# Kernel optimization log

Hardware: AMD Instinct MI355X
Metric: run time of the kernel (lower is better)

Reference implementation:

```python
import jax, jax.numpy as jnp
import numpy as np

WIN = 7  # skimage structural_similarity default win_size


def _uniform_valid(x):
    # x: [N, H, W] -> [N, H-6, W-6]; 7x7 uniform (box) filter, VALID.
    # exactly equivalent to uniform_filter + crop (boundary mode irrelevant).
    k = jnp.ones((1, 1, WIN, WIN), x.dtype) / (WIN * WIN)
    y = jax.lax.conv_general_dilated(x[:, None], k, (1, 1), 'VALID')
    return y[:, 0]


def _ssim_frames(x, y):
    # K1=0.01, K2=0.03, data_range=255, sample covariance (N/(N-1)).
    C1 = (0.01 * 255.0) ** 2
    C2 = (0.03 * 255.0) ** 2
    NP = WIN * WIN
    cov_norm = NP / (NP - 1.0)
    ux = _uniform_valid(x)
    uy = _uniform_valid(y)
    uxx = _uniform_valid(x * x)
    uyy = _uniform_valid(y * y)
    uxy = _uniform_valid(x * y)
    vx = cov_norm * (uxx - ux * ux)
    vy = cov_norm * (uyy - uy * uy)
    vxy = cov_norm * (uxy - ux * uy)
    S = ((2.0 * ux * uy + C1) * (2.0 * vxy + C2)) / (
        (ux * ux + uy * uy + C1) * (vx + vy + C2))
    return jnp.mean(S, axis=(1, 2))  # per-frame mean SSIM


def setup_inputs() -> dict:
    key = jax.random.key(0)
    k1, k2, k3 = jax.random.split(key, 3)
    B, T, C, H, W = 8, 20, 1, 512, 512
    gen_img = jax.random.uniform(k1, (B, T, C, H, W), dtype=jnp.float32)
    target = jax.random.uniform(k2, (B, T, C, H, W), dtype=jnp.float32)
    gen_D = jax.random.normal(k3, (B, 1), dtype=jnp.float32)
    return {"gen_img": gen_img, "target": target, "gen_D": gen_D}


def reference(gen_img, target, gen_D):
    B, T, C, H, W = gen_img.shape
    diff = gen_img - target
    L_rec = jnp.mean(jnp.abs(diff)) + jnp.mean(diff * diff)
    # SSIM on channel 0 of every frame, scaled by 255 (as in the numpy loop);
    # original detaches, so stop_gradient for faithfulness.
    x = gen_img[:, :, 0].reshape(B * T, H, W) * 255.0
    y = target[:, :, 0].reshape(B * T, H, W) * 255.0
    L_ssim = jnp.mean(jax.lax.stop_gradient(_ssim_frames(x, y)))
    L_adv = -jnp.mean(gen_D)
    L_total = L_rec + 0.01 * (1.0 - L_ssim) + 0.0001 * L_adv
    return (L_total, L_rec, L_ssim, L_adv)
```

## Files before the change

### kernel.cpp

```cpp
#include <hip/hip_runtime.h>

#define FRAMES 160
#define HH 512
#define WW 512
#define STRIPS 16
#define NBLK (STRIPS * FRAMES)
#define NTOT 41943040

__device__ __forceinline__ void sync_lds() {
  __builtin_amdgcn_s_waitcnt(0xC07F);
  __builtin_amdgcn_s_barrier();
}

__device__ __forceinline__ float ssim_fast(float a, float b, float sxx,
                                           float syy, float sxy) {
  const float K1 = 0.2401f;
  const float K2 = 2.1609f;
  const float cA = 49.0f / 24.0f;
  const float cB = 49.0f / 48.0f;
  float ab = a * b;
  float s2 = fmaf(a, a, b * b);
  float A1 = fmaf(2.0f, ab, K1);
  float B1 = s2 + K1;
  float A2 = fmaf(cA, fmaf(49.0f, sxy, -ab), K2);
  float B2 = fmaf(cB, fmaf(49.0f, sxx + syy, -s2), K2);
  return (A1 * A2) * __builtin_amdgcn_rcpf(B1 * B2);
}

#define HSTORE(S, P, A)                          \
  P.x = S.x; P.y = P.x + S.y;                    \
  P.z = P.y + S.z; P.w = P.z + S.w;              \
  lds[grp][A][0][q] = make_float2(P.x, P.y);     \
  lds[grp][A][1][q] = make_float2(P.z, P.w);

#define HWIN(P, W, A) {                          \
  float2 h1 = lds[grp][A][1][q + 1];             \
  float2 l2 = lds[grp][A][0][q + 2];             \
  W.x = P.w + h1.x;                              \
  W.y = (P.w - P.x) + h1.y;                      \
  W.z = (P.w - P.y) + (h1.y + l2.x);             \
  W.w = (P.w - P.z) + (h1.y + l2.y); }

#define LREC(xv, yv) {                                         \
  float4 d_ = make_float4(xv.x - yv.x, xv.y - yv.y,            \
                          xv.z - yv.z, xv.w - yv.w);           \
  sabs += fabsf(d_.x) + fabsf(d_.y) + fabsf(d_.z) + fabsf(d_.w); \
  ssq += d_.x * d_.x + d_.y * d_.y;                            \
  ssq += d_.z * d_.z + d_.w * d_.w; }

#define VADD(xv, yv)                                    \
  Sx += xv; Sy += yv;                                   \
  Sxx += xv * xv; Syy += yv * yv; Sxy += xv * yv;

#define VSUB(xv, yv)                                    \
  Sx -= xv; Sy -= yv;                                   \
  Sxx -= xv * xv; Syy -= yv * yv; Sxy -= xv * yv;

__global__ __launch_bounds__(256, 4) void fused_kernel(
    const float* __restrict__ gsrc, const float* __restrict__ tsrc,
    float* __restrict__ ws) {
  const int strip = blockIdx.x;
  const int frame = blockIdx.y;
  const int row0 = strip * 32;
  const int n_iter = (strip == STRIPS - 1) ? 13 : 16;
  const int tid = threadIdx.x;
  const int grp = tid >> 7;
  const int q = tid & 127;

  const float* gp = gsrc + ((size_t)frame * HH + row0 + grp) * WW + q * 4;
  const float* tp = tsrc + ((size_t)frame * HH + row0 + grp) * WW + q * 4;

  __shared__ float2 lds[2][5][2][132];

  float4 Sx = make_float4(0.f, 0.f, 0.f, 0.f);
  float4 Sy = Sx, Sxx = Sx, Syy = Sx, Sxy = Sx;
  float sabs = 0.f, ssq = 0.f, ssum = 0.f;

  for (int i = 0; i < 7; ++i) {
    float4 xv = *(const float4*)(gp + i * WW);
    float4 yv = *(const float4*)(tp + i * WW);
    VADD(xv, yv)
    if (grp == 0) { LREC(xv, yv) }
  }

  for (int it = 0; it < n_iter; ++it) {
    const bool slide = (it + 1 < n_iter);
    float4 nx0, ny0, nx1, ny1, ox0, oy0, ox1, oy1;
    if (slide) {
      const float* pn = gp + (size_t)(2 * it + 7) * WW;
      const float* qn = tp + (size_t)(2 * it + 7) * WW;
      const float* po = gp + (size_t)(2 * it) * WW;
      const float* qo = tp + (size_t)(2 * it) * WW;
      nx0 = *(const float4*)pn;
      ny0 = *(const float4*)qn;
      nx1 = *(const float4*)(pn + WW);
      ny1 = *(const float4*)(qn + WW);
      ox0 = *(const float4*)po;
      oy0 = *(const float4*)qo;
      ox1 = *(const float4*)(po + WW);
      oy1 = *(const float4*)(qo + WW);
    }

    float4 Px, Py, Pxx, Pyy, Pxy;
    HSTORE(Sx, Px, 0) HSTORE(Sy, Py, 1) HSTORE(Sxx, Pxx, 2)
    HSTORE(Syy, Pyy, 3) HSTORE(Sxy, Pxy, 4)
    sync_lds();
    float4 Wx, Wy, Wxx, Wyy, Wxy;
    HWIN(Px, Wx, 0) HWIN(Py, Wy, 1) HWIN(Pxx, Wxx, 2)
    HWIN(Pyy, Wyy, 3) HWIN(Pxy, Wxy, 4)
    float v0 = ssim_fast(Wx.x, Wy.x, Wxx.x, Wyy.x, Wxy.x);
    float v1 = ssim_fast(Wx.y, Wy.y, Wxx.y, Wyy.y, Wxy.y);
    float v2 = ssim_fast(Wx.z, Wy.z, Wxx.z, Wyy.z, Wxy.z);
    float v3 = ssim_fast(Wx.w, Wy.w, Wxx.w, Wyy.w, Wxy.w);
    ssum += (q <= 126) ? v0 : 0.f;
    ssum += (q <= 126) ? v1 : 0.f;
    ssum += (q <= 125) ? v2 : 0.f;
    ssum += (q <= 125) ? v3 : 0.f;
    sync_lds();

    if (slide) {
      VADD(nx0, ny0)
      VSUB(ox0, oy0)
      if ((grp == 0) && (2 * it + 7 <= 30)) { LREC(nx0, ny0) }
      VADD(nx1, ny1)
      VSUB(ox1, oy1)
      bool cnt = (grp == 0) ? (2 * it + 8 <= 30) : (2 * it + 9 == 31);
      if (cnt) { LREC(nx1, ny1) }
    }
  }

  #pragma unroll
  for (int off = 32; off > 0; off >>= 1) {
    sabs += __shfl_down(sabs, off, 64);
    ssq += __shfl_down(ssq, off, 64);
    ssum += __shfl_down(ssum, off, 64);
  }
  __syncthreads();
  float* scr = (float*)&lds[0][0][0][0];
  const int lane = tid & 63, wv = tid >> 6;
  if (lane == 0) { scr[wv] = sabs; scr[4 + wv] = ssq; scr[8 + wv] = ssum; }
  __syncthreads();
  if (tid == 0) {
    const int bid = blockIdx.y * STRIPS + blockIdx.x;
    ws[bid] = scr[0] + scr[1] + scr[2] + scr[3];
    ws[NBLK + bid] = scr[4] + scr[5] + scr[6] + scr[7];
    ws[2 * NBLK + bid] = scr[8] + scr[9] + scr[10] + scr[11];
  }
}

__global__ __launch_bounds__(256) void finalize_kernel(
    const float* __restrict__ ws, const float* __restrict__ genD,
    float* __restrict__ out) {
  const int tid = threadIdx.x;
  float a = 0.f, b = 0.f, c = 0.f;
  for (int i = tid; i < NBLK; i += 256) {
    a += ws[i];
    b += ws[NBLK + i];
    c += ws[2 * NBLK + i];
  }
  #pragma unroll
  for (int off = 32; off > 0; off >>= 1) {
    a += __shfl_down(a, off, 64);
    b += __shfl_down(b, off, 64);
    c += __shfl_down(c, off, 64);
  }
  __shared__ float la[4], lb[4], lc[4];
  const int lane = tid & 63, wv = tid >> 6;
  if (lane == 0) { la[wv] = a; lb[wv] = b; lc[wv] = c; }
  __syncthreads();
  if (tid == 0) {
    a = la[0] + la[1] + la[2] + la[3];
    b = lb[0] + lb[1] + lb[2] + lb[3];
    c = lc[0] + lc[1] + lc[2] + lc[3];
    const float invN = 1.0f / (float)NTOT;
    float L_rec = a * invN + b * invN;
    float L_ssim = c / (160.0f * 506.0f * 506.0f);
    float d = 0.f;
    #pragma unroll
    for (int i = 0; i < 8; ++i) d += genD[i];
    float L_adv = -d / 8.0f;
    float L_total = L_rec + 0.01f * (1.0f - L_ssim) + 0.0001f * L_adv;
    out[0] = L_total;
    out[1] = L_rec;
    out[2] = L_ssim;
    out[3] = L_adv;
  }
}

extern "C" void kernel_launch(void* const* d_in, const int* in_sizes, int n_in,
                              void* d_out, int out_size, void* d_ws,
                              size_t ws_size, hipStream_t stream) {
  const float* gen_img = (const float*)d_in[0];
  const float* target = (const float*)d_in[1];
  const float* gen_D = (const float*)d_in[2];
  float* out = (float*)d_out;
  float* ws = (float*)d_ws;

  dim3 grid(STRIPS, FRAMES);
  fused_kernel<<<grid, 256, 0, stream>>>(gen_img, target, ws);
  finalize_kernel<<<1, 256, 0, stream>>>(ws, gen_D, out);
}
```

Before: 362.9 us.

## Use wave shuffles for horizontal box sums with 8 columns per thread

Each thread now covers 8 columns with a wave of 64 spanning a full row, so the 7-wide horizontal window sums come from prefix sums plus __shfl_down instead of LDS stores, barriers and reloads. Sxx and Syy are merged into a single accumulator and updates use fma. Blocks shrink to 128 threads with two rows each, which removes the per-iteration barriers. In exchange each thread holds more registers, which can lower occupancy, and each thread issues twice as many loads per row.

```diff
diff --git a/kernel.cpp b/kernel.cpp
--- a/kernel.cpp
+++ b/kernel.cpp
@@ -7,13 +7,9 @@
 #define NBLK (STRIPS * FRAMES)
 #define NTOT 41943040
 
-__device__ __forceinline__ void sync_lds() {
-  __builtin_amdgcn_s_waitcnt(0xC07F);
-  __builtin_amdgcn_s_barrier();
-}
-
-__device__ __forceinline__ float ssim_fast(float a, float b, float sxx,
-                                           float syy, float sxy) {
+
+__device__ __forceinline__ float ssim_fast(float a, float b, float sss,
+                                           float sxy) {
   const float K1 = 0.2401f;
   const float K2 = 2.1609f;
   const float cA = 49.0f / 24.0f;
@@ -23,40 +19,66 @@
   float A1 = fmaf(2.0f, ab, K1);
   float B1 = s2 + K1;
   float A2 = fmaf(cA, fmaf(49.0f, sxy, -ab), K2);
-  float B2 = fmaf(cB, fmaf(49.0f, sxx + syy, -s2), K2);
+  float B2 = fmaf(cB, fmaf(49.0f, sss, -s2), K2);
   return (A1 * A2) * __builtin_amdgcn_rcpf(B1 * B2);
 }
 
-#define HSTORE(S, P, A)                          \
-  P.x = S.x; P.y = P.x + S.y;                    \
-  P.z = P.y + S.z; P.w = P.z + S.w;              \
-  lds[grp][A][0][q] = make_float2(P.x, P.y);     \
-  lds[grp][A][1][q] = make_float2(P.z, P.w);
-
-#define HWIN(P, W, A) {                          \
-  float2 h1 = lds[grp][A][1][q + 1];             \
-  float2 l2 = lds[grp][A][0][q + 2];             \
-  W.x = P.w + h1.x;                              \
-  W.y = (P.w - P.x) + h1.y;                      \
-  W.z = (P.w - P.y) + (h1.y + l2.x);             \
-  W.w = (P.w - P.z) + (h1.y + l2.y); }
-
-#define LREC(xv, yv) {                                         \
-  float4 d_ = make_float4(xv.x - yv.x, xv.y - yv.y,            \
-                          xv.z - yv.z, xv.w - yv.w);           \
-  sabs += fabsf(d_.x) + fabsf(d_.y) + fabsf(d_.z) + fabsf(d_.w); \
-  ssq += d_.x * d_.x + d_.y * d_.y;                            \
-  ssq += d_.z * d_.z + d_.w * d_.w; }
-
-#define VADD(xv, yv)                                    \
-  Sx += xv; Sy += yv;                                   \
-  Sxx += xv * xv; Syy += yv * yv; Sxy += xv * yv;
-
-#define VSUB(xv, yv)                                    \
-  Sx -= xv; Sy -= yv;                                   \
-  Sxx -= xv * xv; Syy -= yv * yv; Sxy -= xv * yv;
-
-__global__ __launch_bounds__(256, 4) void fused_kernel(
+#define ACC1(sx, sy, ss, sp, x_, y_)                  \
+  sx += x_; sy += y_;                                 \
+  ss = fmaf(x_, x_, ss); ss = fmaf(y_, y_, ss);       \
+  sp = fmaf(x_, y_, sp);
+
+#define SUB1(sx, sy, ss, sp, x_, y_)                  \
+  sx -= x_; sy -= y_;                                 \
+  ss = fmaf(-x_, x_, ss); ss = fmaf(-y_, y_, ss);     \
+  sp = fmaf(-x_, y_, sp);
+
+#define ACC4(sx, sy, ss, sp, xv, yv)                  \
+  ACC1(sx.x, sy.x, ss.x, sp.x, xv.x, yv.x)            \
+  ACC1(sx.y, sy.y, ss.y, sp.y, xv.y, yv.y)            \
+  ACC1(sx.z, sy.z, ss.z, sp.z, xv.z, yv.z)            \
+  ACC1(sx.w, sy.w, ss.w, sp.w, xv.w, yv.w)
+
+#define SUB4(sx, sy, ss, sp, xv, yv)                  \
+  SUB1(sx.x, sy.x, ss.x, sp.x, xv.x, yv.x)            \
+  SUB1(sx.y, sy.y, ss.y, sp.y, xv.y, yv.y)            \
+  SUB1(sx.z, sy.z, ss.z, sp.z, xv.z, yv.z)            \
+  SUB1(sx.w, sy.w, ss.w, sp.w, xv.w, yv.w)
+
+#define LREC4(xv, yv) {                                         \
+  float d0_ = xv.x - yv.x, d1_ = xv.y - yv.y,                   \
+        d2_ = xv.z - yv.z, d3_ = xv.w - yv.w;                   \
+  sabs += (fabsf(d0_) + fabsf(d1_)) + (fabsf(d2_) + fabsf(d3_)); \
+  ssq = fmaf(d0_, d0_, ssq); ssq = fmaf(d1_, d1_, ssq);         \
+  ssq = fmaf(d2_, d2_, ssq); ssq = fmaf(d3_, d3_, ssq); }
+
+#define HORIZ(lo, hi, dst)                            \
+  {                                                   \
+    float p0 = lo.x;                                  \
+    float p1 = p0 + lo.y;                             \
+    float p2 = p1 + lo.z;                             \
+    float p3 = p2 + lo.w;                             \
+    float p4 = p3 + hi.x;                             \
+    float p5 = p4 + hi.y;                             \
+    float p6 = p5 + hi.z;                             \
+    float p7 = p6 + hi.w;                             \
+    float n0 = __shfl_down(p0, 1, 64);                \
+    float n1 = __shfl_down(p1, 1, 64);                \
+    float n2 = __shfl_down(p2, 1, 64);                \
+    float n3 = __shfl_down(p3, 1, 64);                \
+    float n4 = __shfl_down(p4, 1, 64);                \
+    float n5 = __shfl_down(p5, 1, 64);                \
+    dst[0] = p6;                                      \
+    dst[1] = p7 - p0;                                 \
+    dst[2] = (p7 - p1) + n0;                          \
+    dst[3] = (p7 - p2) + n1;                          \
+    dst[4] = (p7 - p3) + n2;                          \
+    dst[5] = (p7 - p4) + n3;                          \
+    dst[6] = (p7 - p5) + n4;                          \
+    dst[7] = (p7 - p6) + n5;                          \
+  }
+
+__global__ __launch_bounds__(128, 3) void fused_kernel(
     const float* __restrict__ gsrc, const float* __restrict__ tsrc,
     float* __restrict__ ws) {
   const int strip = blockIdx.x;
@@ -64,68 +86,82 @@
   const int row0 = strip * 32;
   const int n_iter = (strip == STRIPS - 1) ? 13 : 16;
   const int tid = threadIdx.x;
-  const int grp = tid >> 7;
-  const int q = tid & 127;
-
-  const float* gp = gsrc + ((size_t)frame * HH + row0 + grp) * WW + q * 4;
-  const float* tp = tsrc + ((size_t)frame * HH + row0 + grp) * WW + q * 4;
-
-  __shared__ float2 lds[2][5][2][132];
-
-  float4 Sx = make_float4(0.f, 0.f, 0.f, 0.f);
-  float4 Sy = Sx, Sxx = Sx, Syy = Sx, Sxy = Sx;
+  const int grp = tid >> 6;
+  const int q = tid & 63;
+
+  const float* gp = gsrc + ((size_t)frame * HH + row0 + grp) * WW + q * 8;
+  const float* tp = tsrc + ((size_t)frame * HH + row0 + grp) * WW + q * 8;
+
+  const float4 z4 = make_float4(0.f, 0.f, 0.f, 0.f);
+  float4 Sx0 = z4, Sx1 = z4, Sy0 = z4, Sy1 = z4;
+  float4 Ss0 = z4, Ss1 = z4, Sp0 = z4, Sp1 = z4;
   float sabs = 0.f, ssq = 0.f, ssum = 0.f;
 
+  #pragma unroll
   for (int i = 0; i < 7; ++i) {
-    float4 xv = *(const float4*)(gp + i * WW);
-    float4 yv = *(const float4*)(tp + i * WW);
-    VADD(xv, yv)
-    if (grp == 0) { LREC(xv, yv) }
-  }
-
+    float4 xa = *(const float4*)(gp + (size_t)i * WW);
+    float4 xb = *(const float4*)(gp + (size_t)i * WW + 4);
+    float4 ya = *(const float4*)(tp + (size_t)i * WW);
+    float4 yb = *(const float4*)(tp + (size_t)i * WW + 4);
+    ACC4(Sx0, Sy0, Ss0, Sp0, xa, ya)
+    ACC4(Sx1, Sy1, Ss1, Sp1, xb, yb)
+    if (grp == 0) { LREC4(xa, ya) LREC4(xb, yb) }
+  }
+
+  #pragma unroll 1
   for (int it = 0; it < n_iter; ++it) {
     const bool slide = (it + 1 < n_iter);
-    float4 nx0, ny0, nx1, ny1, ox0, oy0, ox1, oy1;
+    float4 nx0a, nx0b, ny0a, ny0b, nx1a, nx1b, ny1a, ny1b;
+    float4 ox0a, ox0b, oy0a, oy0b, ox1a, ox1b, oy1a, oy1b;
     if (slide) {
       const float* pn = gp + (size_t)(2 * it + 7) * WW;
       const float* qn = tp + (size_t)(2 * it + 7) * WW;
       const float* po = gp + (size_t)(2 * it) * WW;
       const float* qo = tp + (size_t)(2 * it) * WW;
-      nx0 = *(const float4*)pn;
-      ny0 = *(const float4*)qn;
-      nx1 = *(const float4*)(pn + WW);
-      ny1 = *(const float4*)(qn + WW);
-      ox0 = *(const float4*)po;
-      oy0 = *(const float4*)qo;
-      ox1 = *(const float4*)(po + WW);
-      oy1 = *(const float4*)(qo + WW);
+      nx0a = *(const float4*)pn;
+      nx0b = *(const float4*)(pn + 4);
+      ny0a = *(const float4*)qn;
+      ny0b = *(const float4*)(qn + 4);
+      nx1a = *(const float4*)(pn + WW);
+      nx1b = *(const float4*)(pn + WW + 4);
+      ny1a = *(const float4*)(qn + WW);
+      ny1b = *(const float4*)(qn + WW + 4);
+      ox0a = *(const float4*)po;
+      ox0b = *(const float4*)(po + 4);
+      oy0a = *(const float4*)qo;
+      oy0b = *(const float4*)(qo + 4);
+      ox1a = *(const float4*)(po + WW);
+      ox1b = *(const float4*)(po + WW + 4);
+      oy1a = *(const float4*)(qo + WW);
+      oy1b = *(const float4*)(qo + WW + 4);
     }
 
-    float4 Px, Py, Pxx, Pyy, Pxy;
-    HSTORE(Sx, Px, 0) HSTORE(Sy, Py, 1) HSTORE(Sxx, Pxx, 2)
-    HSTORE(Syy, Pyy, 3) HSTORE(Sxy, Pxy, 4)
-    sync_lds();
-    float4 Wx, Wy, Wxx, Wyy, Wxy;
-    HWIN(Px, Wx, 0) HWIN(Py, Wy, 1) HWIN(Pxx, Wxx, 2)
-    HWIN(Pyy, Wyy, 3) HWIN(Pxy, Wxy, 4)
-    float v0 = ssim_fast(Wx.x, Wy.x, Wxx.x, Wyy.x, Wxy.x);
-    float v1 = ssim_fast(Wx.y, Wy.y, Wxx.y, Wyy.y, Wxy.y);
-    float v2 = ssim_fast(Wx.z, Wy.z, Wxx.z, Wyy.z, Wxy.z);
-    float v3 = ssim_fast(Wx.w, Wy.w, Wxx.w, Wyy.w, Wxy.w);
-    ssum += (q <= 126) ? v0 : 0.f;
-    ssum += (q <= 126) ? v1 : 0.f;
-    ssum += (q <= 125) ? v2 : 0.f;
-    ssum += (q <= 125) ? v3 : 0.f;
-    sync_lds();
+    float wx[8], wy[8], wss[8], wxy[8];
+    HORIZ(Sx0, Sx1, wx)
+    HORIZ(Sy0, Sy1, wy)
+    HORIZ(Ss0, Ss1, wss)
+    HORIZ(Sp0, Sp1, wxy)
+
+    float v[8];
+    #pragma unroll
+    for (int j = 0; j < 8; ++j)
+      v[j] = ssim_fast(wx[j], wy[j], wss[j], wxy[j]);
+    ssum += v[0] + v[1];
+    float vr = ((v[2] + v[3]) + (v[4] + v[5])) + (v[6] + v[7]);
+    ssum += (q < 63) ? vr : 0.f;
 
     if (slide) {
-      VADD(nx0, ny0)
-      VSUB(ox0, oy0)
-      if ((grp == 0) && (2 * it + 7 <= 30)) { LREC(nx0, ny0) }
-      VADD(nx1, ny1)
-      VSUB(ox1, oy1)
+      ACC4(Sx0, Sy0, Ss0, Sp0, nx0a, ny0a)
+      ACC4(Sx1, Sy1, Ss1, Sp1, nx0b, ny0b)
+      SUB4(Sx0, Sy0, Ss0, Sp0, ox0a, oy0a)
+      SUB4(Sx1, Sy1, Ss1, Sp1, ox0b, oy0b)
+      if ((grp == 0) && (2 * it + 7 <= 30)) { LREC4(nx0a, ny0a) LREC4(nx0b, ny0b) }
+      ACC4(Sx0, Sy0, Ss0, Sp0, nx1a, ny1a)
+      ACC4(Sx1, Sy1, Ss1, Sp1, nx1b, ny1b)
+      SUB4(Sx0, Sy0, Ss0, Sp0, ox1a, oy1a)
+      SUB4(Sx1, Sy1, Ss1, Sp1, ox1b, oy1b)
       bool cnt = (grp == 0) ? (2 * it + 8 <= 30) : (2 * it + 9 == 31);
-      if (cnt) { LREC(nx1, ny1) }
+      if (cnt) { LREC4(nx1a, ny1a) LREC4(nx1b, ny1b) }
     }
   }
 
@@ -135,16 +171,14 @@
     ssq += __shfl_down(ssq, off, 64);
     ssum += __shfl_down(ssum, off, 64);
   }
-  __syncthreads();
-  float* scr = (float*)&lds[0][0][0][0];
-  const int lane = tid & 63, wv = tid >> 6;
-  if (lane == 0) { scr[wv] = sabs; scr[4 + wv] = ssq; scr[8 + wv] = ssum; }
+  __shared__ float scr[6];
+  if (q == 0) { scr[grp] = sabs; scr[2 + grp] = ssq; scr[4 + grp] = ssum; }
   __syncthreads();
   if (tid == 0) {
     const int bid = blockIdx.y * STRIPS + blockIdx.x;
-    ws[bid] = scr[0] + scr[1] + scr[2] + scr[3];
-    ws[NBLK + bid] = scr[4] + scr[5] + scr[6] + scr[7];
-    ws[2 * NBLK + bid] = scr[8] + scr[9] + scr[10] + scr[11];
+    ws[bid] = scr[0] + scr[1];
+    ws[NBLK + bid] = scr[2] + scr[3];
+    ws[2 * NBLK + bid] = scr[4] + scr[5];
   }
 }
 
@@ -197,6 +231,6 @@
   float* ws = (float*)d_ws;
 
   dim3 grid(STRIPS, FRAMES);
-  fused_kernel<<<grid, 256, 0, stream>>>(gen_img, target, ws);
+  fused_kernel<<<grid, 128, 0, stream>>>(gen_img, target, ws);
   finalize_kernel<<<1, 256, 0, stream>>>(ws, gen_D, out);
 }
```

Result: slower. 463.7 us (+27.8%).
